# Performance work log

Hardware: AMD Instinct MI355X
Metric: run time of the kernel (lower is better)

The kernel has to match this reference:

```python
import jax, jax.numpy as jnp
import numpy as np

NUM_EXPERTS = 8
TOP_K = 2
HIDDEN = 2048
INTER = 7168
B, S = 4, 2048


def setup_inputs() -> dict:
    key = jax.random.key(0)
    k0, k1, k2, k3, k4 = jax.random.split(key, 5)
    scale_h = 1.0 / np.sqrt(HIDDEN)
    scale_i = 1.0 / np.sqrt(INTER)
    return {
        "hidden_states": jax.random.normal(k0, (B, S, HIDDEN), dtype=jnp.float32),
        "gate_w": jax.random.normal(k1, (NUM_EXPERTS, HIDDEN), dtype=jnp.float32) * scale_h,
        "w1": jax.random.normal(k2, (NUM_EXPERTS, INTER, HIDDEN), dtype=jnp.float32) * scale_h,
        "w3": jax.random.normal(k3, (NUM_EXPERTS, INTER, HIDDEN), dtype=jnp.float32) * scale_h,
        "w2": jax.random.normal(k4, (NUM_EXPERTS, HIDDEN, INTER), dtype=jnp.float32) * scale_i,
    }


def reference(hidden_states, gate_w, w1, w3, w2):
    orig_shape = hidden_states.shape
    x = hidden_states.reshape(-1, HIDDEN)              # [T, H]

    # Router: gate linear -> softmax -> top-k -> renormalize.
    router_logits = x @ gate_w.T                       # [T, E]
    probs = jax.nn.softmax(router_logits, axis=-1)
    topk_w, topk_idx = jax.lax.top_k(probs, TOP_K)     # [T, K]
    topk_w = topk_w / jnp.sum(topk_w, axis=-1, keepdims=True)

    # Dense combine weights: [T, E] with top-k renormalized weights scattered.
    combine = jnp.sum(
        jax.nn.one_hot(topk_idx, NUM_EXPERTS, dtype=x.dtype) * topk_w[..., None],
        axis=1,
    )                                                   # [T, E]

    out = jnp.zeros_like(x)
    # Fixed small loop over experts (structurally distinct weight matrices);
    # avoids materializing a [T, E, I] intermediate.
    for e in range(NUM_EXPERTS):
        g = jax.nn.silu(x @ w1[e].T)                   # [T, I]
        u = x @ w3[e].T                                # [T, I]
        y = (g * u) @ w2[e].T                          # [T, H]
        out = out + combine[:, e:e + 1] * y

    return out.reshape(orig_shape)
```

## Files before the change

### kernel.cpp

```cpp
#include <hip/hip_runtime.h>
#include <stdint.h>

#define NE    8
#define HID   2048
#define INTER 7168
#define TTOK  8192
#define NT1   (HID / 64)
#define NT2   (INTER / 64)

typedef __bf16 bf16;
typedef bf16 bf16x4 __attribute__((ext_vector_type(4)));
typedef bf16 bf16x8 __attribute__((ext_vector_type(8)));
typedef float f32x4 __attribute__((ext_vector_type(4)));

__device__ __forceinline__ void glds16(const void* g, void* l) {
  __builtin_amdgcn_global_load_lds((__attribute__((address_space(1))) void*)g,
                                   (__attribute__((address_space(3))) void*)l, 16, 0, 0);
}

__global__ void cvt_f32_bf16(const float* __restrict__ src, bf16* __restrict__ dst, long n) {
  long i = (long)blockIdx.x * blockDim.x + threadIdx.x;
  long stride = (long)gridDim.x * blockDim.x;
  for (long j = i * 4; j < n; j += stride * 4) {
    float4 v = *(const float4*)(src + j);
    bf16x4 o = {(bf16)v.x, (bf16)v.y, (bf16)v.z, (bf16)v.w};
    *(bf16x4*)(dst + j) = o;
  }
}

__global__ void router_kernel(const float* __restrict__ x, const float* __restrict__ gw,
                              int* __restrict__ topk_e, float* __restrict__ topk_w) {
  const int wid = threadIdx.x >> 6, lane = threadIdx.x & 63;
  const int t = blockIdx.x * 4 + wid;
  if (t >= TTOK) return;
  const float* xr = x + (size_t)t * HID;
  float xv[32];
#pragma unroll
  for (int i = 0; i < 32; ++i) xv[i] = xr[lane + 64 * i];
  float lg[NE];
#pragma unroll
  for (int e = 0; e < NE; ++e) {
    const float* g = gw + e * HID;
    float s = 0.f;
#pragma unroll
    for (int i = 0; i < 32; ++i) s += xv[i] * g[lane + 64 * i];
#pragma unroll
    for (int off = 32; off; off >>= 1) s += __shfl_down(s, off);
    lg[e] = s;
  }
  if (lane == 0) {
    int i1 = 0;
#pragma unroll
    for (int e = 1; e < NE; ++e) if (lg[e] > lg[i1]) i1 = e;
    int i2 = (i1 == 0) ? 1 : 0;
#pragma unroll
    for (int e = 0; e < NE; ++e) if (e != i2 && e != i1 && lg[e] > lg[i2]) i2 = e;
    float r = __expf(lg[i2] - lg[i1]);
    float wa = 1.f / (1.f + r);
    topk_e[2 * t] = i1; topk_e[2 * t + 1] = i2;
    topk_w[2 * t] = wa; topk_w[2 * t + 1] = 1.f - wa;
  }
}

__global__ void gather_kernel(const int* __restrict__ topk_e, const float* __restrict__ topk_w,
                              int* __restrict__ cnt, int* __restrict__ ltok, float* __restrict__ lw) {
  const int t = blockIdx.x * blockDim.x + threadIdx.x;
  if (t >= TTOK) return;
#pragma unroll
  for (int j = 0; j < 2; ++j) {
    int e = topk_e[2 * t + j];
    int s = atomicAdd(&cnt[e], 1);
    ltok[e * TTOK + s] = t;
    lw[e * TTOK + s] = topk_w[2 * t + j];
  }
}

__global__ void prefix_kernel(const int* __restrict__ cnt, int* __restrict__ base) {
  if (threadIdx.x == 0 && blockIdx.x == 0) {
    int b = 0;
    for (int e = 0; e < NE; ++e) { base[e] = b; b += cnt[e]; }
  }
}


#define MFMA(a, b, c) __builtin_amdgcn_mfma_f32_16x16x32_bf16((a), (b), (c), 0, 0, 0)

#define STAGE_A(h, kt) do { int _b = ((kt) & 1) * 32768; size_t _k = (size_t)(kt) * 128; \
    glds16(bA + oA[(h)*2 + 0] + _k, ldsA + _b + (h) * 16384 + d0); \
    glds16(bA + oA[(h)*2 + 1] + _k, ldsA + _b + (h) * 16384 + d1); } while (0)
#define STAGE_B(h, kt) do { int _b = ((kt) & 1) * 32768; size_t _k = (size_t)(kt) * 128; \
    glds16(bB + oB[(h)*2 + 0] + _k, ldsB + _b + (h) * 16384 + d0); \
    glds16(bB + oB[(h)*2 + 1] + _k, ldsB + _b + (h) * 16384 + d1); } while (0)

#define RD_A(mf, ks) (*(const bf16x8*)(ldsA + curb + arow + (mf) * (16 * 128) + ((ks) ? kcol1 : kcol0)))
#define RD_B(nf, ks) (*(const bf16x8*)(ldsB + curb + brow + (nf) * (16 * 128) + ((ks) ? kcol1 : kcol0)))

#define BAR()   __builtin_amdgcn_s_barrier()
#define LGKM0() do { asm volatile("s_waitcnt lgkmcnt(0)" ::: "memory"); \
                     __builtin_amdgcn_sched_barrier(0); } while (0)

__launch_bounds__(512, 2)
__global__ void pass1_kernel(const bf16* __restrict__ xb, const bf16* __restrict__ w1b,
                             bf16* __restrict__ hbuf, const int* __restrict__ cnt,
                             const int* __restrict__ basep, const int* __restrict__ ltok) {
  const int e = blockIdx.z;
  const int c = cnt[e];
  const int tm = blockIdx.y;
  if (tm * 256 >= c) return;
  const int tn = blockIdx.x;

  __shared__ __align__(16) bf16 sA[2][256 * 64];
  __shared__ __align__(16) bf16 sB[2][256 * 64];
  char* const ldsA = (char*)&sA[0][0];
  char* const ldsB = (char*)&sB[0][0];

  const int tid = threadIdx.x;
  const int r0 = tid >> 3;
  const int ls = (tid & 7) ^ (r0 & 7);
  const int d0 = tid * 16, d1 = (tid + 512) * 16;
  const char* const bA = (const char*)xb;
  const char* const bB = (const char*)w1b;

  uint32_t oA[4], oB[4];
#pragma unroll
  for (int i = 0; i < 4; ++i) {
    int trow = i * 64 + r0;
    int slot = tm * 256 + trow; if (slot >= c) slot = c - 1;
    oA[i] = (uint32_t)((size_t)ltok[e * TTOK + slot] * (HID * 2) + ls * 16);
    int br = i * 64 + r0;
    int w = (br >> 4) & 1;
    int wr = tn * 128 + ((br >> 5) << 4) + (br & 15);
    size_t off = ((size_t)e * INTER + wr) * (HID * 2) + (size_t)ls * 16;
    if (w) off += (size_t)NE * INTER * HID * 2;
    oB[i] = (uint32_t)off;
  }

  const int lane = tid & 63, wid = tid >> 6;
  const int wm = wid >> 2, wn = wid & 3;
  const int ln15 = lane & 15, kq = lane >> 4;
  const int swz = (ln15 & 7) << 4;
  const int kcol0 = (kq * 16) ^ swz;
  const int kcol1 = (64 + kq * 16) ^ swz;
  const int arow = (wm * 128 + ln15) * 128;
  const int brow = (wn * 64 + ln15) * 128;

  f32x4 acc[8][4];
#pragma unroll
  for (int m = 0; m < 8; ++m)
#pragma unroll
    for (int n = 0; n < 4; ++n) acc[m][n] = (f32x4){0.f, 0.f, 0.f, 0.f};

  STAGE_A(0, 0); STAGE_A(1, 0); STAGE_B(0, 0); STAGE_B(1, 0);
  asm volatile("s_waitcnt vmcnt(4)" ::: "memory");
  STAGE_A(0, 1); STAGE_A(1, 1); STAGE_B(0, 1);
  asm volatile("s_waitcnt vmcnt(6)" ::: "memory");
  BAR();

  bf16x8 a0[4][2], a1[4][2], b0[2][2], b1[2][2];
  int cur = 0;
  for (int t = 0; t < NT1; ++t, cur ^= 1) {
    const int curb = cur * 32768;
#pragma unroll
    for (int m = 0; m < 4; ++m) { a0[m][0] = RD_A(m, 0); a0[m][1] = RD_A(m, 1); }
#pragma unroll
    for (int n = 0; n < 2; ++n) { b0[n][0] = RD_B(n, 0); b0[n][1] = RD_B(n, 1); }
    if (t + 1 < NT1) STAGE_B(1, t + 1);
    BAR(); LGKM0();
    __builtin_amdgcn_s_setprio(1);
#pragma unroll
    for (int m = 0; m < 4; ++m)
#pragma unroll
      for (int n = 0; n < 2; ++n) {
        acc[m][n] = MFMA(a0[m][0], b0[n][0], acc[m][n]);
        acc[m][n] = MFMA(a0[m][1], b0[n][1], acc[m][n]);
      }
    __builtin_amdgcn_s_setprio(0);
    BAR();
#pragma unroll
    for (int m = 0; m < 4; ++m) { a1[m][0] = RD_A(4 + m, 0); a1[m][1] = RD_A(4 + m, 1); }
    if (t + 2 < NT1) STAGE_A(0, t + 2);
    BAR(); LGKM0();
    __builtin_amdgcn_s_setprio(1);
#pragma unroll
    for (int m = 0; m < 4; ++m)
#pragma unroll
      for (int n = 0; n < 2; ++n) {
        acc[4 + m][n] = MFMA(a1[m][0], b0[n][0], acc[4 + m][n]);
        acc[4 + m][n] = MFMA(a1[m][1], b0[n][1], acc[4 + m][n]);
      }
    __builtin_amdgcn_s_setprio(0);
    BAR();
#pragma unroll
    for (int n = 0; n < 2; ++n) { b1[n][0] = RD_B(2 + n, 0); b1[n][1] = RD_B(2 + n, 1); }
    if (t + 2 < NT1) STAGE_A(1, t + 2);
    BAR(); LGKM0();
    __builtin_amdgcn_s_setprio(1);
#pragma unroll
    for (int m = 0; m < 4; ++m)
#pragma unroll
      for (int n = 0; n < 2; ++n) {
        acc[m][2 + n] = MFMA(a0[m][0], b1[n][0], acc[m][2 + n]);
        acc[m][2 + n] = MFMA(a0[m][1], b1[n][1], acc[m][2 + n]);
      }
    __builtin_amdgcn_s_setprio(0);
    BAR();
    if (t + 2 < NT1) STAGE_B(0, t + 2);
    __builtin_amdgcn_s_setprio(1);
#pragma unroll
    for (int m = 0; m < 4; ++m)
#pragma unroll
      for (int n = 0; n < 2; ++n) {
        acc[4 + m][2 + n] = MFMA(a1[m][0], b1[n][0], acc[4 + m][2 + n]);
        acc[4 + m][2 + n] = MFMA(a1[m][1], b1[n][1], acc[4 + m][2 + n]);
      }
    __builtin_amdgcn_s_setprio(0);
    if (t + 2 < NT1) asm volatile("s_waitcnt vmcnt(6)" ::: "memory");
    else             asm volatile("s_waitcnt vmcnt(0)" ::: "memory");
    BAR();
  }

  const int be = basep[e];
#pragma unroll
  for (int mh = 0; mh < 2; ++mh)
#pragma unroll
    for (int mf = 0; mf < 4; ++mf)
#pragma unroll
      for (int j = 0; j < 4; ++j) {
        const int slot = tm * 256 + wm * 128 + mh * 64 + mf * 16 + kq * 4 + j;
        if (slot < c) {
          bf16* hrow = hbuf + (size_t)(be + slot) * INTER + tn * 128;
#pragma unroll
          for (int p = 0; p < 2; ++p) {
            const float g = acc[mh * 4 + mf][2 * p][j];
            const float u = acc[mh * 4 + mf][2 * p + 1][j];
            const float hv = g / (1.f + __expf(-g)) * u;
            hrow[wn * 32 + p * 16 + ln15] = (bf16)hv;
          }
        }
      }
}

__launch_bounds__(512, 2)
__global__ void pass2_kernel(const bf16* __restrict__ hbuf, const bf16* __restrict__ w2b,
                             float* __restrict__ out, const int* __restrict__ cnt,
                             const int* __restrict__ basep, const int* __restrict__ ltok,
                             const float* __restrict__ lw) {
  const int e = blockIdx.z;
  const int c = cnt[e];
  const int tm = blockIdx.y;
  if (tm * 256 >= c) return;
  const int tn = blockIdx.x;

  __shared__ __align__(16) bf16 sA[2][256 * 64];
  __shared__ __align__(16) bf16 sB[2][256 * 64];
  char* const ldsA = (char*)&sA[0][0];
  char* const ldsB = (char*)&sB[0][0];

  const int tid = threadIdx.x;
  const int r0 = tid >> 3;
  const int ls = (tid & 7) ^ (r0 & 7);
  const int d0 = tid * 16, d1 = (tid + 512) * 16;
  const int be = basep[e];
  const char* const bA = (const char*)hbuf;
  const char* const bB = (const char*)w2b;

  uint32_t oA[4], oB[4];
#pragma unroll
  for (int i = 0; i < 4; ++i) {
    int trow = i * 64 + r0;
    int slot = tm * 256 + trow; if (slot >= c) slot = c - 1;
    oA[i] = (uint32_t)((size_t)(be + slot) * (INTER * 2) + ls * 16);
    int br = i * 64 + r0;
    oB[i] = (uint32_t)(((size_t)e * HID + tn * 256 + br) * (INTER * 2) + (size_t)ls * 16);
  }

  const int lane = tid & 63, wid = tid >> 6;
  const int wm = wid >> 2, wn = wid & 3;
  const int ln15 = lane & 15, kq = lane >> 4;
  const int swz = (ln15 & 7) << 4;
  const int kcol0 = (kq * 16) ^ swz;
  const int kcol1 = (64 + kq * 16) ^ swz;
  const int arow = (wm * 128 + ln15) * 128;
  const int brow = (wn * 64 + ln15) * 128;

  f32x4 acc[8][4];
#pragma unroll
  for (int m = 0; m < 8; ++m)
#pragma unroll
    for (int n = 0; n < 4; ++n) acc[m][n] = (f32x4){0.f, 0.f, 0.f, 0.f};

  STAGE_A(0, 0); STAGE_A(1, 0); STAGE_B(0, 0); STAGE_B(1, 0);
  asm volatile("s_waitcnt vmcnt(4)" ::: "memory");
  STAGE_A(0, 1); STAGE_A(1, 1); STAGE_B(0, 1);
  asm volatile("s_waitcnt vmcnt(6)" ::: "memory");
  BAR();

  bf16x8 a0[4][2], a1[4][2], b0[2][2], b1[2][2];
  int cur = 0;
  for (int t = 0; t < NT2; ++t, cur ^= 1) {
    const int curb = cur * 32768;
#pragma unroll
    for (int m = 0; m < 4; ++m) { a0[m][0] = RD_A(m, 0); a0[m][1] = RD_A(m, 1); }
#pragma unroll
    for (int n = 0; n < 2; ++n) { b0[n][0] = RD_B(n, 0); b0[n][1] = RD_B(n, 1); }
    if (t + 1 < NT2) STAGE_B(1, t + 1);
    BAR(); LGKM0();
    __builtin_amdgcn_s_setprio(1);
#pragma unroll
    for (int m = 0; m < 4; ++m)
#pragma unroll
      for (int n = 0; n < 2; ++n) {
        acc[m][n] = MFMA(a0[m][0], b0[n][0], acc[m][n]);
        acc[m][n] = MFMA(a0[m][1], b0[n][1], acc[m][n]);
      }
    __builtin_amdgcn_s_setprio(0);
    BAR();
#pragma unroll
    for (int m = 0; m < 4; ++m) { a1[m][0] = RD_A(4 + m, 0); a1[m][1] = RD_A(4 + m, 1); }
    if (t + 2 < NT2) STAGE_A(0, t + 2);
    BAR(); LGKM0();
    __builtin_amdgcn_s_setprio(1);
#pragma unroll
    for (int m = 0; m < 4; ++m)
#pragma unroll
      for (int n = 0; n < 2; ++n) {
        acc[4 + m][n] = MFMA(a1[m][0], b0[n][0], acc[4 + m][n]);
        acc[4 + m][n] = MFMA(a1[m][1], b0[n][1], acc[4 + m][n]);
      }
    __builtin_amdgcn_s_setprio(0);
    BAR();
#pragma unroll
    for (int n = 0; n < 2; ++n) { b1[n][0] = RD_B(2 + n, 0); b1[n][1] = RD_B(2 + n, 1); }
    if (t + 2 < NT2) STAGE_A(1, t + 2);
    BAR(); LGKM0();
    __builtin_amdgcn_s_setprio(1);
#pragma unroll
    for (int m = 0; m < 4; ++m)
#pragma unroll
      for (int n = 0; n < 2; ++n) {
        acc[m][2 + n] = MFMA(a0[m][0], b1[n][0], acc[m][2 + n]);
        acc[m][2 + n] = MFMA(a0[m][1], b1[n][1], acc[m][2 + n]);
      }
    __builtin_amdgcn_s_setprio(0);
    BAR();
    if (t + 2 < NT2) STAGE_B(0, t + 2);
    __builtin_amdgcn_s_setprio(1);
#pragma unroll
    for (int m = 0; m < 4; ++m)
#pragma unroll
      for (int n = 0; n < 2; ++n) {
        acc[4 + m][2 + n] = MFMA(a1[m][0], b1[n][0], acc[4 + m][2 + n]);
        acc[4 + m][2 + n] = MFMA(a1[m][1], b1[n][1], acc[4 + m][2 + n]);
      }
    __builtin_amdgcn_s_setprio(0);
    if (t + 2 < NT2) asm volatile("s_waitcnt vmcnt(6)" ::: "memory");
    else             asm volatile("s_waitcnt vmcnt(0)" ::: "memory");
    BAR();
  }

#pragma unroll
  for (int mh = 0; mh < 2; ++mh)
#pragma unroll
    for (int mf = 0; mf < 4; ++mf)
#pragma unroll
      for (int j = 0; j < 4; ++j) {
        const int slot = tm * 256 + wm * 128 + mh * 64 + mf * 16 + kq * 4 + j;
        if (slot < c) {
          const int tok = ltok[e * TTOK + slot];
          const float wt = lw[e * TTOK + slot];
          float* orow = out + (size_t)tok * HID + tn * 256;
#pragma unroll
          for (int n = 0; n < 4; ++n)
            atomicAdd(orow + wn * 64 + n * 16 + ln15, wt * acc[mh * 4 + mf][n][j]);
        }
      }
}

extern "C" void kernel_launch(void* const* d_in, const int* in_sizes, int n_in,
                              void* d_out, int out_size, void* d_ws, size_t ws_size,
                              hipStream_t stream) {
  const float* x  = (const float*)d_in[0];
  const float* gw = (const float*)d_in[1];
  const float* w1 = (const float*)d_in[2];
  const float* w3 = (const float*)d_in[3];
  const float* w2 = (const float*)d_in[4];
  float* out = (float*)d_out;

  char* ws = (char*)d_ws;
  size_t off = 0;
  auto take = [&](size_t bytes) -> char* {
    char* p = ws + off;
    off += (bytes + 255) & ~(size_t)255;
    return p;
  };
  bf16* xb    = (bf16*)take((size_t)TTOK * HID * 2);
  bf16* w1b   = (bf16*)take((size_t)NE * INTER * HID * 2);
  bf16* w3b   = (bf16*)take((size_t)NE * INTER * HID * 2);
  bf16* w2b   = (bf16*)take((size_t)NE * HID * INTER * 2);
  bf16* hbuf  = (bf16*)take((size_t)TTOK * 2 * INTER * 2);
  int*   topk_e = (int*)take(TTOK * 2 * 4);
  float* topk_w = (float*)take(TTOK * 2 * 4);
  int*   ltok   = (int*)take(NE * TTOK * 4);
  float* lwgt   = (float*)take(NE * TTOK * 4);
  int*   cntp   = (int*)take(64);
  int*   basep  = (int*)take(64);
  if (off > ws_size) return;

  hipMemsetAsync(d_out, 0, (size_t)out_size * 4, stream);
  hipMemsetAsync(cntp, 0, 64, stream);

  cvt_f32_bf16<<<2048, 256, 0, stream>>>(x,  xb,  (long)TTOK * HID);
  cvt_f32_bf16<<<4096, 256, 0, stream>>>(w1, w1b, (long)NE * INTER * HID);
  cvt_f32_bf16<<<4096, 256, 0, stream>>>(w3, w3b, (long)NE * INTER * HID);
  cvt_f32_bf16<<<4096, 256, 0, stream>>>(w2, w2b, (long)NE * HID * INTER);

  router_kernel<<<TTOK / 4, 256, 0, stream>>>(x, gw, topk_e, topk_w);
  gather_kernel<<<TTOK / 256, 256, 0, stream>>>(topk_e, topk_w, cntp, ltok, lwgt);
  prefix_kernel<<<1, 64, 0, stream>>>(cntp, basep);

  pass1_kernel<<<dim3(INTER / 128, TTOK / 256, NE), 512, 0, stream>>>(
      xb, w1b, hbuf, cntp, basep, ltok);
  pass2_kernel<<<dim3(HID / 256, TTOK / 256, NE), 512, 0, stream>>>(
      hbuf, w2b, out, cntp, basep, ltok, lwgt);
}
```

Measured before the change: 2.292 ms.

## Switch expert GEMMs to 32x32x16 MFMA with restructured LDS read schedule

Replaces the 16x16x32 bf16 MFMA tiles with 32x32x16 MFMA in both the gate/up and down-projection kernels, regrouping per-wave accumulators into 4x2 blocks of 32x32. The K-loop is reorganized into two half-phases with fewer barriers, and three of the four next-stage global-to-LDS loads are issued together. The W1/W3 interleave in the B tile and the epilogue indexing change to match the 32x32 output layout. The larger MFMA should cut LDS read traffic per flop and instruction count, at the cost of changed prefetch overlap and register pressure.

```diff
diff --git a/kernel.cpp b/kernel.cpp
--- a/kernel.cpp
+++ b/kernel.cpp
@@ -11,7 +11,7 @@
 typedef __bf16 bf16;
 typedef bf16 bf16x4 __attribute__((ext_vector_type(4)));
 typedef bf16 bf16x8 __attribute__((ext_vector_type(8)));
-typedef float f32x4 __attribute__((ext_vector_type(4)));
+typedef float f32x16 __attribute__((ext_vector_type(16)));
 
 __device__ __forceinline__ void glds16(const void* g, void* l) {
   __builtin_amdgcn_global_load_lds((__attribute__((address_space(1))) void*)g,
@@ -83,7 +83,7 @@
 }
 
 
-#define MFMA(a, b, c) __builtin_amdgcn_mfma_f32_16x16x32_bf16((a), (b), (c), 0, 0, 0)
+#define MFMA32(a, b, c) __builtin_amdgcn_mfma_f32_32x32x16_bf16((a), (b), (c), 0, 0, 0)
 
 #define STAGE_A(h, kt) do { int _b = ((kt) & 1) * 32768; size_t _k = (size_t)(kt) * 128; \
     glds16(bA + oA[(h)*2 + 0] + _k, ldsA + _b + (h) * 16384 + d0); \
@@ -92,12 +92,13 @@
     glds16(bB + oB[(h)*2 + 0] + _k, ldsB + _b + (h) * 16384 + d0); \
     glds16(bB + oB[(h)*2 + 1] + _k, ldsB + _b + (h) * 16384 + d1); } while (0)
 
-#define RD_A(mf, ks) (*(const bf16x8*)(ldsA + curb + arow + (mf) * (16 * 128) + ((ks) ? kcol1 : kcol0)))
-#define RD_B(nf, ks) (*(const bf16x8*)(ldsB + curb + brow + (nf) * (16 * 128) + ((ks) ? kcol1 : kcol0)))
+#define RD_A(mf, ks) (*(const bf16x8*)(ldsA + curb + arow + (mf) * 4096 + kcol[ks]))
+#define RD_B(nf, ks) (*(const bf16x8*)(ldsB + curb + brow + (nf) * 4096 + kcol[ks]))
 
 #define BAR()   __builtin_amdgcn_s_barrier()
 #define LGKM0() do { asm volatile("s_waitcnt lgkmcnt(0)" ::: "memory"); \
                      __builtin_amdgcn_sched_barrier(0); } while (0)
+#define SCHED0() __builtin_amdgcn_sched_barrier(0)
 
 __launch_bounds__(512, 2)
 __global__ void pass1_kernel(const bf16* __restrict__ xb, const bf16* __restrict__ w1b,
@@ -127,92 +128,73 @@
     int trow = i * 64 + r0;
     int slot = tm * 256 + trow; if (slot >= c) slot = c - 1;
     oA[i] = (uint32_t)((size_t)ltok[e * TTOK + slot] * (HID * 2) + ls * 16);
-    int br = i * 64 + r0;
-    int w = (br >> 4) & 1;
-    int wr = tn * 128 + ((br >> 5) << 4) + (br & 15);
+    int wr = tn * 128 + i * 32 + (r0 & 31);
     size_t off = ((size_t)e * INTER + wr) * (HID * 2) + (size_t)ls * 16;
-    if (w) off += (size_t)NE * INTER * HID * 2;
+    if (r0 >> 5) off += (size_t)NE * INTER * HID * 2;
     oB[i] = (uint32_t)off;
   }
 
   const int lane = tid & 63, wid = tid >> 6;
   const int wm = wid >> 2, wn = wid & 3;
-  const int ln15 = lane & 15, kq = lane >> 4;
-  const int swz = (ln15 & 7) << 4;
-  const int kcol0 = (kq * 16) ^ swz;
-  const int kcol1 = (64 + kq * 16) ^ swz;
-  const int arow = (wm * 128 + ln15) * 128;
-  const int brow = (wn * 64 + ln15) * 128;
-
-  f32x4 acc[8][4];
-#pragma unroll
-  for (int m = 0; m < 8; ++m)
-#pragma unroll
-    for (int n = 0; n < 4; ++n) acc[m][n] = (f32x4){0.f, 0.f, 0.f, 0.f};
+  const int ln31 = lane & 31, kq2 = lane >> 5;
+  const int swz = (ln31 & 7) << 4;
+  int kcol[4];
+#pragma unroll
+  for (int ks = 0; ks < 4; ++ks) kcol[ks] = (ks * 32 + kq2 * 16) ^ swz;
+  const int arow = (wm * 128 + ln31) * 128;
+  const int brow = (wn * 64 + ln31) * 128;
+
+  f32x16 acc[4][2];
+#pragma unroll
+  for (int m = 0; m < 4; ++m)
+#pragma unroll
+    for (int n = 0; n < 2; ++n) acc[m][n] = (f32x16)(0.f);
 
   STAGE_A(0, 0); STAGE_A(1, 0); STAGE_B(0, 0); STAGE_B(1, 0);
-  asm volatile("s_waitcnt vmcnt(4)" ::: "memory");
   STAGE_A(0, 1); STAGE_A(1, 1); STAGE_B(0, 1);
   asm volatile("s_waitcnt vmcnt(6)" ::: "memory");
   BAR();
 
-  bf16x8 a0[4][2], a1[4][2], b0[2][2], b1[2][2];
+  bf16x8 aF[2][4], bF[2][4];
   int cur = 0;
   for (int t = 0; t < NT1; ++t, cur ^= 1) {
     const int curb = cur * 32768;
 #pragma unroll
-    for (int m = 0; m < 4; ++m) { a0[m][0] = RD_A(m, 0); a0[m][1] = RD_A(m, 1); }
-#pragma unroll
-    for (int n = 0; n < 2; ++n) { b0[n][0] = RD_B(n, 0); b0[n][1] = RD_B(n, 1); }
-    if (t + 1 < NT1) STAGE_B(1, t + 1);
-    BAR(); LGKM0();
+    for (int m = 0; m < 2; ++m)
+#pragma unroll
+      for (int ks = 0; ks < 4; ++ks) aF[m][ks] = RD_A(m, ks);
+#pragma unroll
+    for (int n = 0; n < 2; ++n)
+#pragma unroll
+      for (int ks = 0; ks < 4; ++ks) bF[n][ks] = RD_B(n, ks);
+    LGKM0();
+    BAR();
+    if (t + 1 < NT1) { STAGE_B(1, t + 1); SCHED0(); }
     __builtin_amdgcn_s_setprio(1);
 #pragma unroll
-    for (int m = 0; m < 4; ++m)
-#pragma unroll
-      for (int n = 0; n < 2; ++n) {
-        acc[m][n] = MFMA(a0[m][0], b0[n][0], acc[m][n]);
-        acc[m][n] = MFMA(a0[m][1], b0[n][1], acc[m][n]);
-      }
+    for (int ks = 0; ks < 4; ++ks)
+#pragma unroll
+      for (int m = 0; m < 2; ++m)
+#pragma unroll
+        for (int n = 0; n < 2; ++n)
+          acc[m][n] = MFMA32(aF[m][ks], bF[n][ks], acc[m][n]);
     __builtin_amdgcn_s_setprio(0);
     BAR();
 #pragma unroll
-    for (int m = 0; m < 4; ++m) { a1[m][0] = RD_A(4 + m, 0); a1[m][1] = RD_A(4 + m, 1); }
-    if (t + 2 < NT1) STAGE_A(0, t + 2);
-    BAR(); LGKM0();
+    for (int m = 0; m < 2; ++m)
+#pragma unroll
+      for (int ks = 0; ks < 4; ++ks) aF[m][ks] = RD_A(2 + m, ks);
+    LGKM0();
+    BAR();
+    if (t + 2 < NT1) { STAGE_A(0, t + 2); STAGE_A(1, t + 2); STAGE_B(0, t + 2); SCHED0(); }
     __builtin_amdgcn_s_setprio(1);
 #pragma unroll
-    for (int m = 0; m < 4; ++m)
-#pragma unroll
-      for (int n = 0; n < 2; ++n) {
-        acc[4 + m][n] = MFMA(a1[m][0], b0[n][0], acc[4 + m][n]);
-        acc[4 + m][n] = MFMA(a1[m][1], b0[n][1], acc[4 + m][n]);
-      }
-    __builtin_amdgcn_s_setprio(0);
-    BAR();
-#pragma unroll
-    for (int n = 0; n < 2; ++n) { b1[n][0] = RD_B(2 + n, 0); b1[n][1] = RD_B(2 + n, 1); }
-    if (t + 2 < NT1) STAGE_A(1, t + 2);
-    BAR(); LGKM0();
-    __builtin_amdgcn_s_setprio(1);
-#pragma unroll
-    for (int m = 0; m < 4; ++m)
-#pragma unroll
-      for (int n = 0; n < 2; ++n) {
-        acc[m][2 + n] = MFMA(a0[m][0], b1[n][0], acc[m][2 + n]);
-        acc[m][2 + n] = MFMA(a0[m][1], b1[n][1], acc[m][2 + n]);
-      }
-    __builtin_amdgcn_s_setprio(0);
-    BAR();
-    if (t + 2 < NT1) STAGE_B(0, t + 2);
-    __builtin_amdgcn_s_setprio(1);
-#pragma unroll
-    for (int m = 0; m < 4; ++m)
-#pragma unroll
-      for (int n = 0; n < 2; ++n) {
-        acc[4 + m][2 + n] = MFMA(a1[m][0], b1[n][0], acc[4 + m][2 + n]);
-        acc[4 + m][2 + n] = MFMA(a1[m][1], b1[n][1], acc[4 + m][2 + n]);
-      }
+    for (int ks = 0; ks < 4; ++ks)
+#pragma unroll
+      for (int m = 0; m < 2; ++m)
+#pragma unroll
+        for (int n = 0; n < 2; ++n)
+          acc[2 + m][n] = MFMA32(aF[m][ks], bF[n][ks], acc[2 + m][n]);
     __builtin_amdgcn_s_setprio(0);
     if (t + 2 < NT1) asm volatile("s_waitcnt vmcnt(6)" ::: "memory");
     else             asm volatile("s_waitcnt vmcnt(0)" ::: "memory");
@@ -220,24 +202,20 @@
   }
 
   const int be = basep[e];
-#pragma unroll
-  for (int mh = 0; mh < 2; ++mh)
-#pragma unroll
-    for (int mf = 0; mf < 4; ++mf)
-#pragma unroll
-      for (int j = 0; j < 4; ++j) {
-        const int slot = tm * 256 + wm * 128 + mh * 64 + mf * 16 + kq * 4 + j;
-        if (slot < c) {
-          bf16* hrow = hbuf + (size_t)(be + slot) * INTER + tn * 128;
-#pragma unroll
-          for (int p = 0; p < 2; ++p) {
-            const float g = acc[mh * 4 + mf][2 * p][j];
-            const float u = acc[mh * 4 + mf][2 * p + 1][j];
-            const float hv = g / (1.f + __expf(-g)) * u;
-            hrow[wn * 32 + p * 16 + ln15] = (bf16)hv;
-          }
-        }
+  const int hcol = tn * 128 + wn * 32 + ln31;
+#pragma unroll
+  for (int mf = 0; mf < 4; ++mf)
+#pragma unroll
+    for (int reg = 0; reg < 16; ++reg) {
+      const int row = mf * 32 + (reg & 3) + 8 * (reg >> 2) + 4 * kq2;
+      const int slot = tm * 256 + wm * 128 + row;
+      if (slot < c) {
+        const float g = acc[mf][0][reg];
+        const float u = acc[mf][1][reg];
+        const float hv = g / (1.f + __expf(-g)) * u;
+        hbuf[(size_t)(be + slot) * INTER + hcol] = (bf16)hv;
       }
+    }
 }
 
 __launch_bounds__(512, 2)
@@ -270,88 +248,70 @@
     int trow = i * 64 + r0;
     int slot = tm * 256 + trow; if (slot >= c) slot = c - 1;
     oA[i] = (uint32_t)((size_t)(be + slot) * (INTER * 2) + ls * 16);
-    int br = i * 64 + r0;
-    oB[i] = (uint32_t)(((size_t)e * HID + tn * 256 + br) * (INTER * 2) + (size_t)ls * 16);
+    oB[i] = (uint32_t)(((size_t)e * HID + tn * 256 + i * 64 + r0) * (INTER * 2) + (size_t)ls * 16);
   }
 
   const int lane = tid & 63, wid = tid >> 6;
   const int wm = wid >> 2, wn = wid & 3;
-  const int ln15 = lane & 15, kq = lane >> 4;
-  const int swz = (ln15 & 7) << 4;
-  const int kcol0 = (kq * 16) ^ swz;
-  const int kcol1 = (64 + kq * 16) ^ swz;
-  const int arow = (wm * 128 + ln15) * 128;
-  const int brow = (wn * 64 + ln15) * 128;
-
-  f32x4 acc[8][4];
-#pragma unroll
-  for (int m = 0; m < 8; ++m)
-#pragma unroll
-    for (int n = 0; n < 4; ++n) acc[m][n] = (f32x4){0.f, 0.f, 0.f, 0.f};
+  const int ln31 = lane & 31, kq2 = lane >> 5;
+  const int swz = (ln31 & 7) << 4;
+  int kcol[4];
+#pragma unroll
+  for (int ks = 0; ks < 4; ++ks) kcol[ks] = (ks * 32 + kq2 * 16) ^ swz;
+  const int arow = (wm * 128 + ln31) * 128;
+  const int brow = (wn * 64 + ln31) * 128;
+
+  f32x16 acc[4][2];
+#pragma unroll
+  for (int m = 0; m < 4; ++m)
+#pragma unroll
+    for (int n = 0; n < 2; ++n) acc[m][n] = (f32x16)(0.f);
 
   STAGE_A(0, 0); STAGE_A(1, 0); STAGE_B(0, 0); STAGE_B(1, 0);
-  asm volatile("s_waitcnt vmcnt(4)" ::: "memory");
   STAGE_A(0, 1); STAGE_A(1, 1); STAGE_B(0, 1);
   asm volatile("s_waitcnt vmcnt(6)" ::: "memory");
   BAR();
 
-  bf16x8 a0[4][2], a1[4][2], b0[2][2], b1[2][2];
+  bf16x8 aF[2][4], bF[2][4];
   int cur = 0;
   for (int t = 0; t < NT2; ++t, cur ^= 1) {
     const int curb = cur * 32768;
 #pragma unroll
-    for (int m = 0; m < 4; ++m) { a0[m][0] = RD_A(m, 0); a0[m][1] = RD_A(m, 1); }
-#pragma unroll
-    for (int n = 0; n < 2; ++n) { b0[n][0] = RD_B(n, 0); b0[n][1] = RD_B(n, 1); }
-    if (t + 1 < NT2) STAGE_B(1, t + 1);
-    BAR(); LGKM0();
+    for (int m = 0; m < 2; ++m)
+#pragma unroll
+      for (int ks = 0; ks < 4; ++ks) aF[m][ks] = RD_A(m, ks);
+#pragma unroll
+    for (int n = 0; n < 2; ++n)
+#pragma unroll
+      for (int ks = 0; ks < 4; ++ks) bF[n][ks] = RD_B(n, ks);
+    LGKM0();
+    BAR();
+    if (t + 1 < NT2) { STAGE_B(1, t + 1); SCHED0(); }
     __builtin_amdgcn_s_setprio(1);
 #pragma unroll
-    for (int m = 0; m < 4; ++m)
-#pragma unroll
-      for (int n = 0; n < 2; ++n) {
-        acc[m][n] = MFMA(a0[m][0], b0[n][0], acc[m][n]);
-        acc[m][n] = MFMA(a0[m][1], b0[n][1], acc[m][n]);
-      }
+    for (int ks = 0; ks < 4; ++ks)
+#pragma unroll
+      for (int m = 0; m < 2; ++m)
+#pragma unroll
+        for (int n = 0; n < 2; ++n)
+          acc[m][n] = MFMA32(aF[m][ks], bF[n][ks], acc[m][n]);
     __builtin_amdgcn_s_setprio(0);
     BAR();
 #pragma unroll
-    for (int m = 0; m < 4; ++m) { a1[m][0] = RD_A(4 + m, 0); a1[m][1] = RD_A(4 + m, 1); }
-    if (t + 2 < NT2) STAGE_A(0, t + 2);
-    BAR(); LGKM0();
+    for (int m = 0; m < 2; ++m)
+#pragma unroll
+      for (int ks = 0; ks < 4; ++ks) aF[m][ks] = RD_A(2 + m, ks);
+    LGKM0();
+    BAR();
+    if (t + 2 < NT2) { STAGE_A(0, t + 2); STAGE_A(1, t + 2); STAGE_B(0, t + 2); SCHED0(); }
     __builtin_amdgcn_s_setprio(1);
 #pragma unroll
-    for (int m = 0; m < 4; ++m)
-#pragma unroll
-      for (int n = 0; n < 2; ++n) {
-        acc[4 + m][n] = MFMA(a1[m][0], b0[n][0], acc[4 + m][n]);
-        acc[4 + m][n] = MFMA(a1[m][1], b0[n][1], acc[4 + m][n]);
-      }
-    __builtin_amdgcn_s_setprio(0);
-    BAR();
-#pragma unroll
-    for (int n = 0; n < 2; ++n) { b1[n][0] = RD_B(2 + n, 0); b1[n][1] = RD_B(2 + n, 1); }
-    if (t + 2 < NT2) STAGE_A(1, t + 2);
-    BAR(); LGKM0();
-    __builtin_amdgcn_s_setprio(1);
-#pragma unroll
-    for (int m = 0; m < 4; ++m)
-#pragma unroll
-      for (int n = 0; n < 2; ++n) {
-        acc[m][2 + n] = MFMA(a0[m][0], b1[n][0], acc[m][2 + n]);
-        acc[m][2 + n] = MFMA(a0[m][1], b1[n][1], acc[m][2 + n]);
-      }
-    __builtin_amdgcn_s_setprio(0);
-    BAR();
-    if (t + 2 < NT2) STAGE_B(0, t + 2);
-    __builtin_amdgcn_s_setprio(1);
-#pragma unroll
-    for (int m = 0; m < 4; ++m)
-#pragma unroll
-      for (int n = 0; n < 2; ++n) {
-        acc[4 + m][2 + n] = MFMA(a1[m][0], b1[n][0], acc[4 + m][2 + n]);
-        acc[4 + m][2 + n] = MFMA(a1[m][1], b1[n][1], acc[4 + m][2 + n]);
-      }
+    for (int ks = 0; ks < 4; ++ks)
+#pragma unroll
+      for (int m = 0; m < 2; ++m)
+#pragma unroll
+        for (int n = 0; n < 2; ++n)
+          acc[2 + m][n] = MFMA32(aF[m][ks], bF[n][ks], acc[2 + m][n]);
     __builtin_amdgcn_s_setprio(0);
     if (t + 2 < NT2) asm volatile("s_waitcnt vmcnt(6)" ::: "memory");
     else             asm volatile("s_waitcnt vmcnt(0)" ::: "memory");
@@ -359,21 +319,20 @@
   }
 
 #pragma unroll
-  for (int mh = 0; mh < 2; ++mh)
-#pragma unroll
-    for (int mf = 0; mf < 4; ++mf)
-#pragma unroll
-      for (int j = 0; j < 4; ++j) {
-        const int slot = tm * 256 + wm * 128 + mh * 64 + mf * 16 + kq * 4 + j;
-        if (slot < c) {
-          const int tok = ltok[e * TTOK + slot];
-          const float wt = lw[e * TTOK + slot];
-          float* orow = out + (size_t)tok * HID + tn * 256;
-#pragma unroll
-          for (int n = 0; n < 4; ++n)
-            atomicAdd(orow + wn * 64 + n * 16 + ln15, wt * acc[mh * 4 + mf][n][j]);
-        }
+  for (int mf = 0; mf < 4; ++mf)
+#pragma unroll
+    for (int reg = 0; reg < 16; ++reg) {
+      const int row = mf * 32 + (reg & 3) + 8 * (reg >> 2) + 4 * kq2;
+      const int slot = tm * 256 + wm * 128 + row;
+      if (slot < c) {
+        const int tok = ltok[e * TTOK + slot];
+        const float wt = lw[e * TTOK + slot];
+        float* orow = out + (size_t)tok * HID + tn * 256 + wn * 64;
+#pragma unroll
+        for (int nf = 0; nf < 2; ++nf)
+          atomicAdd(orow + nf * 32 + ln31, wt * acc[mf][nf][reg]);
       }
+    }
 }
 
 extern "C" void kernel_launch(void* const* d_in, const int* in_sizes, int n_in,
```

Measured after the change: 2.627 ms. +14.6%, slower.
